# Kernel optimization log

Measured on AMD Instinct MI355X. Metric: run time of the kernel, lower is better.

Reference implementation:

```python
import jax, jax.numpy as jnp
import numpy as np

N = 100000      # nodes per type
E = 1600000     # edges per edge type
D = 128         # input feature dim
C = 128         # hidden channels (heads=1, concat)
DE = 16         # edge feature dim
OUT = 64        # out channels
L = 2           # num conv layers
T = 2           # num edge types: 0 = user->item, 1 = item->user


def setup_inputs() -> dict:
    key = jax.random.key(0)
    ks = jax.random.split(key, 17)
    s = 0.05  # keep attention logits / activations well-scaled
    return {
        "x_user": jax.random.normal(ks[0], (N, D), jnp.float32),
        "x_item": jax.random.normal(ks[1], (N, D), jnp.float32),
        "ea_ui": jax.random.normal(ks[2], (E, DE), jnp.float32),
        "ea_iu": jax.random.normal(ks[3], (E, DE), jnp.float32),
        "W_src": jax.random.normal(ks[4], (L, T, C, C), jnp.float32) * s,
        "W_dst": jax.random.normal(ks[5], (L, T, C, C), jnp.float32) * s,
        "W_edge": jax.random.normal(ks[6], (L, T, DE, C), jnp.float32) * s,
        "att_src": jax.random.normal(ks[7], (L, T, C), jnp.float32) * s,
        "att_dst": jax.random.normal(ks[8], (L, T, C), jnp.float32) * s,
        "att_edge": jax.random.normal(ks[9], (L, T, C), jnp.float32) * s,
        "conv_bias": jax.random.normal(ks[10], (L, T, C), jnp.float32) * s,
        "lin0_W": jax.random.normal(ks[11], (2, C, C), jnp.float32) * s,
        "lin0_b": jax.random.normal(ks[12], (2, C), jnp.float32) * s,
        "lin1_W": jax.random.normal(ks[13], (2, C, OUT), jnp.float32) * s,
        "lin1_b": jax.random.normal(ks[14], (2, OUT), jnp.float32) * s,
        "ei_ui": jax.random.randint(ks[15], (2, E), 0, N, jnp.int32),
        "ei_iu": jax.random.randint(ks[16], (2, E), 0, N, jnp.int32),
    }


def _gat_conv(x_src, x_dst, ei, ea, Ws, Wd, We, a_s, a_d, a_e, b):
    """PyG GATConv((-1,-1), C, heads=1, edge_dim=DE, add_self_loops=False)."""
    row, col = ei[0], ei[1]
    hs = x_src @ Ws                      # [Ns, C]
    hd = x_dst @ Wd                      # [Nd, C]
    he = ea @ We                         # [E, C]
    a = hs @ a_s                         # [Ns] alpha_src per source node
    adst = hd @ a_d                      # [Nd] alpha_dst per dest node
    ae = he @ a_e                        # [E]
    alpha = jax.nn.leaky_relu(a[row] + adst[col] + ae, 0.2)  # [E]
    n_dst = x_dst.shape[0]
    m = jax.ops.segment_max(alpha, col, num_segments=n_dst)  # stable softmax max
    ex = jnp.exp(alpha - m[col])
    den = jax.ops.segment_sum(ex, col, num_segments=n_dst)
    w = ex / den[col]                    # edge-softmax over incoming edges
    out = jax.ops.segment_sum(w[:, None] * hs[row], col, num_segments=n_dst)
    return out + b                       # [Nd, C]


def reference(x_user, x_item, ea_ui, ea_iu, W_src, W_dst, W_edge, att_src,
              att_dst, att_edge, conv_bias, lin0_W, lin0_b, lin1_W, lin1_b,
              ei_ui, ei_iu):
    xu, xi = x_user, x_item
    for l in range(L):
        # edge type 0: user -> item ; edge type 1: item -> user
        new_item = _gat_conv(xu, xi, ei_ui, ea_ui, W_src[l, 0], W_dst[l, 0],
                             W_edge[l, 0], att_src[l, 0], att_dst[l, 0],
                             att_edge[l, 0], conv_bias[l, 0])
        new_user = _gat_conv(xi, xu, ei_iu, ea_iu, W_src[l, 1], W_dst[l, 1],
                             W_edge[l, 1], att_src[l, 1], att_dst[l, 1],
                             att_edge[l, 1], conv_bias[l, 1])
        # HeteroConv aggr='sum' has one contribution per dst type; then relu
        xu = jax.nn.relu(new_user)
        xi = jax.nn.relu(new_item)
    # HeteroDictLinear stack (no activation between, per gnn.Sequential spec)
    xu = (xu @ lin0_W[0] + lin0_b[0]) @ lin1_W[0] + lin1_b[0]
    xi = (xi @ lin0_W[1] + lin0_b[1]) @ lin1_W[1] + lin1_b[1]
    return xu, xi
```

## Files before the change

### kernel.cpp

```cpp
#include <hip/hip_runtime.h>
#include <hip/hip_fp16.h>


typedef _Float16 half4 __attribute__((ext_vector_type(4)));
typedef float f32x4 __attribute__((ext_vector_type(4)));

#define KCAP 48

__device__ __forceinline__ float wave_sum(float v){
#pragma unroll
  for (int off = 32; off; off >>= 1) v += __shfl_xor(v, off);
  return v;
}

__global__ __launch_bounds__(64) void precompute_vec_kernel(
    const float* __restrict__ Wsrc, const float* __restrict__ Wdst,
    const float* __restrict__ Wedge, const float* __restrict__ As,
    const float* __restrict__ Ad, const float* __restrict__ Ae,
    float* __restrict__ pv_as, float* __restrict__ pv_ad, float* __restrict__ pv_ae)
{
  int b = blockIdx.x;
  int lt = b / 272, rem = b - lt * 272;
  int lane = threadIdx.x;
  const float* W; const float* a; float* out;
  if (rem < 128)      { W = Wsrc  + lt*16384 + rem*128;       a = As + lt*128; out = pv_as + lt*128 + rem; }
  else if (rem < 256) { int d = rem-128; W = Wdst + lt*16384 + d*128; a = Ad + lt*128; out = pv_ad + lt*128 + d; }
  else                { int j = rem-256; W = Wedge + lt*2048 + j*128; a = Ae + lt*128; out = pv_ae + lt*16 + j; }
  float s = W[lane]*a[lane] + W[lane+64]*a[lane+64];
  s = wave_sum(s);
  if (lane == 0) *out = s;
}

__global__ void combine_linear_kernel(const float* __restrict__ lin0W, const float* __restrict__ lin0b,
                                      const float* __restrict__ lin1W, const float* __restrict__ lin1b,
                                      float* __restrict__ Wc, float* __restrict__ bc)
{
  int idx = blockIdx.x * 256 + threadIdx.x;
  if (idx < 2*128*64) {
    int t = idx / 8192; int r = (idx / 64) & 127; int o = idx & 63;
    const float* w0 = lin0W + t*16384 + r*128;
    const float* w1 = lin1W + t*8192 + o;
    float s = 0.f;
    for (int m = 0; m < 128; ++m) s += w0[m] * w1[m*64];
    Wc[idx] = s;
  } else if (idx < 2*128*64 + 128) {
    int q = idx - 16384; int t = q >> 6; int o = q & 63;
    const float* b0 = lin0b + t*128;
    const float* w1 = lin1W + t*8192 + o;
    float s = lin1b[t*64 + o];
    for (int m = 0; m < 128; ++m) s += b0[m] * w1[m*64];
    bc[q] = s;
  }
}

__global__ __launch_bounds__(256) void wfrag_prep_kernel(
    const float* __restrict__ Wsrc, const float* __restrict__ pv_as,
    const float* __restrict__ pv_ad, const float* __restrict__ Wc,
    _Float16* __restrict__ Wf_conv, _Float16* __restrict__ Wf_mlp)
{
  int idx = blockIdx.x * 256 + threadIdx.x;
  if (idx < 73728) {
    int within = idx & 255;
    int l = within >> 2, i = within & 3;
    int rest = idx >> 8;
    int c = rest % 9; int rest2 = rest / 9;
    int s = rest2 & 7; int g = rest2 >> 3;
    int lg = g >> 1, who = g & 1;
    int k = s*16 + ((l>>4)<<2) + i;
    float val = 0.f;
    if (c < 8) {
      int col = c*16 + (l & 15);
      int lt = lg*2 + who;
      val = Wsrc[(size_t)lt*16384 + k*128 + col];
    } else {
      int cc = l & 15;
      if (cc == 0)      val = pv_as[(lg*2 + who)*128 + k];
      else if (cc == 1) val = pv_ad[(lg*2 + (who^1))*128 + k];
    }
    Wf_conv[idx] = (_Float16)val;
  } else {
    int q = idx - 73728;
    int within = q & 255;
    int l = within >> 2, i = within & 3;
    int rest = q >> 8;
    int c = rest & 3; int s = (rest >> 2) & 7; int m = rest >> 5;
    int k = s*16 + ((l>>4)<<2) + i;
    int col = c*16 + (l & 15);
    Wf_mlp[q] = (_Float16)Wc[m*8192 + k*64 + col];
  }
}

__device__ __forceinline__ void fill_body(
    int fid, int tid,
    const int* __restrict__ ei0, const int* __restrict__ ei1,
    const float* __restrict__ ea0, const float* __restrict__ ea1,
    const float* __restrict__ pv_ae,
    int* __restrict__ cnt0, int* __restrict__ cnt1,
    uint2* __restrict__ bkt0, uint2* __restrict__ bkt1, int E, int gEf)
{
  int type = (fid >= gEf) ? 1 : 0;
  const int* ei = type ? ei1 : ei0;
  const float* ea = type ? ea1 : ea0;
  int* cnt = type ? cnt1 : cnt0;
  uint2* bkt = type ? bkt1 : bkt0;
  int e = (fid - type * gEf) * 256 + tid;
  if (e >= E) return;
  int src = ei[e], col = ei[E + e];
  const float4* er = (const float4*)(ea + (size_t)e * 16);
  float4 a0 = er[0], a1 = er[1], a2 = er[2], a3 = er[3];
  const float* v0 = pv_ae + type * 16;
  const float* v1 = pv_ae + (2 + type) * 16;
  float ae0 = a0.x*v0[0] + a0.y*v0[1] + a0.z*v0[2] + a0.w*v0[3]
            + a1.x*v0[4] + a1.y*v0[5] + a1.z*v0[6] + a1.w*v0[7]
            + a2.x*v0[8] + a2.y*v0[9] + a2.z*v0[10] + a2.w*v0[11]
            + a3.x*v0[12] + a3.y*v0[13] + a3.z*v0[14] + a3.w*v0[15];
  float ae1 = a0.x*v1[0] + a0.y*v1[1] + a0.z*v1[2] + a0.w*v1[3]
            + a1.x*v1[4] + a1.y*v1[5] + a1.z*v1[6] + a1.w*v1[7]
            + a2.x*v1[8] + a2.y*v1[9] + a2.z*v1[10] + a2.w*v1[11]
            + a3.x*v1[12] + a3.y*v1[13] + a3.z*v1[14] + a3.w*v1[15];
  int pos = atomicAdd(&cnt[col], 1);
  if (pos < KCAP) {
    __half2 hh = __floats2half2_rn(ae0, ae1);
    uint2 val;
    val.x = (unsigned)src;
    val.y = *(const unsigned*)&hh;
    bkt[(size_t)col * KCAP + pos] = val;
  }
}

template<bool FIN, bool CONV>
__device__ __forceinline__ void gemm_body(_Float16* ldsb, int blk, int t,
    const void* __restrict__ Xv, const uint2* __restrict__ Wf,
    void* __restrict__ Hout, float* __restrict__ asrc, float* __restrict__ adst,
    const float* __restrict__ bias, int N)
{
  constexpr int NT = CONV ? 9 : 4;
  const int r0 = blk * 64;

  if (FIN) {
    const float* X = (const float*)Xv;
    for (int v = t; v < 2048; v += 256) {
      int row = v >> 5, q = v & 31;
      int r = r0 + row;
      float4 xv = make_float4(0.f, 0.f, 0.f, 0.f);
      if (r < N) xv = *(const float4*)(X + (size_t)r * 128 + q * 4);
      _Float16* d = &ldsb[row * 136 + q * 4];
      d[0] = (_Float16)xv.x; d[1] = (_Float16)xv.y;
      d[2] = (_Float16)xv.z; d[3] = (_Float16)xv.w;
    }
  } else {
    const _Float16* X = (const _Float16*)Xv;
    for (int v = t; v < 1024; v += 256) {
      int row = v >> 4, q = v & 15;
      int r = r0 + row;
      uint4 xv = make_uint4(0u, 0u, 0u, 0u);
      if (r < N) xv = *(const uint4*)(X + (size_t)r * 128 + q * 8);
      *(uint4*)(&ldsb[row * 136 + q * 8]) = xv;
    }
  }
  __syncthreads();

  const int w = t >> 6, l = t & 63;
  f32x4 acc[NT];
#pragma unroll
  for (int c = 0; c < NT; ++c) acc[c] = (f32x4)(0.f);

  const uint2* wp = Wf + l;
  const int aoff = (w * 16 + (l & 15)) * 136 + ((l >> 4) << 2);
#pragma unroll
  for (int s = 0; s < 8; ++s) {
    half4 af = *(const half4*)(&ldsb[aoff + s * 16]);
#pragma unroll
    for (int c = 0; c < NT; ++c) {
      uint2 bw = wp[(s * NT + c) * 64];
      half4 bf = *reinterpret_cast<const half4*>(&bw);
      acc[c] = __builtin_amdgcn_mfma_f32_16x16x16f16(af, bf, acc[c], 0, 0, 0);
    }
  }
  __syncthreads();

  if (CONV) {
#pragma unroll
    for (int c = 0; c < 8; ++c)
#pragma unroll
      for (int rg = 0; rg < 4; ++rg)
        ldsb[(w*16 + ((l>>4)<<2) + rg) * 136 + c*16 + (l & 15)] = (_Float16)acc[c][rg];
    if ((l & 15) < 2) {
      float* dst = ((l & 15) == 0) ? asrc : adst;
#pragma unroll
      for (int rg = 0; rg < 4; ++rg) {
        int r = r0 + w*16 + ((l>>4)<<2) + rg;
        if (r < N) dst[r] = acc[8][rg];
      }
    }
    __syncthreads();
    _Float16* H = (_Float16*)Hout;
    for (int v = t; v < 1024; v += 256) {
      int row = v >> 4, q = v & 15;
      int r = r0 + row;
      if (r < N)
        *(uint4*)(H + (size_t)r * 128 + q * 8) = *(const uint4*)(&ldsb[row * 136 + q * 8]);
    }
  } else {
    float* ldsf = (float*)ldsb;
#pragma unroll
    for (int c = 0; c < 4; ++c)
#pragma unroll
      for (int rg = 0; rg < 4; ++rg)
        ldsf[(w*16 + ((l>>4)<<2) + rg) * 68 + c*16 + (l & 15)] = acc[c][rg];
    __syncthreads();
    float* O = (float*)Hout;
    for (int v = t; v < 1024; v += 256) {
      int row = v >> 4, q = v & 15;
      int r = r0 + row;
      if (r < N) {
        float4 o = *(const float4*)(&ldsf[row * 68 + q * 4]);
        float4 bb = *(const float4*)(bias + q * 4);
        o.x += bb.x; o.y += bb.y; o.z += bb.z; o.w += bb.w;
        *(float4*)(O + (size_t)r * 64 + q * 4) = o;
      }
    }
  }
}

__global__ __launch_bounds__(256) void phase0_kernel(
    const float* __restrict__ xu, const float* __restrict__ xi,
    const uint2* __restrict__ Wfc,
    _Float16* __restrict__ hs_u, _Float16* __restrict__ hs_i,
    float* __restrict__ asrc_u, float* __restrict__ adst_u,
    float* __restrict__ asrc_i, float* __restrict__ adst_i,
    const int* __restrict__ ei0, const int* __restrict__ ei1,
    const float* __restrict__ ea0, const float* __restrict__ ea1,
    const float* __restrict__ pv_ae,
    int* __restrict__ cnt0, int* __restrict__ cnt1,
    uint2* __restrict__ bkt0, uint2* __restrict__ bkt1,
    int N, int E, int gB, int P, int gEf)
{
  __shared__ __align__(16) _Float16 ldsb[64 * 136];
  int b = blockIdx.x, t = threadIdx.x;
  int g = b / P, r = b - g * P;
  if (r == 0) {
    if (g < gB)
      gemm_body<true, true>(ldsb, g, t, xu, Wfc, hs_u, asrc_u, adst_u, nullptr, N);
    else
      gemm_body<true, true>(ldsb, g - gB, t, xi, Wfc + 4608, hs_i, asrc_i, adst_i, nullptr, N);
  } else {
    int fid = b - g - 1;
    if (fid < 2 * gEf)
      fill_body(fid, t, ei0, ei1, ea0, ea1, pv_ae, cnt0, cnt1, bkt0, bkt1, E, gEf);
  }
}

template<bool FIN, bool CONV>
__global__ __launch_bounds__(256) void gemm_pair_kernel(
    const void* __restrict__ X0, const void* __restrict__ X1,
    const uint2* __restrict__ Wf0, const uint2* __restrict__ Wf1,
    void* __restrict__ H0, void* __restrict__ H1,
    float* __restrict__ asrc0, float* __restrict__ adst0,
    float* __restrict__ asrc1, float* __restrict__ adst1,
    const float* __restrict__ bias0, const float* __restrict__ bias1,
    int N, int gB)
{
  __shared__ __align__(16) _Float16 ldsb[64 * 136];
  int b = blockIdx.x;
  if (b < gB)
    gemm_body<FIN, CONV>(ldsb, b, threadIdx.x, X0, Wf0, H0, asrc0, adst0, bias0, N);
  else
    gemm_body<FIN, CONV>(ldsb, b - gB, threadIdx.x, X1, Wf1, H1, asrc1, adst1, bias1, N);
}

__global__ __launch_bounds__(256) void aggregate_pair(
    const int* __restrict__ cnt0, const uint2* __restrict__ bkt0,
    const float* __restrict__ asrc0, const float* __restrict__ adst0,
    const __half2* __restrict__ hs0, const float* __restrict__ bias0,
    __half2* __restrict__ out0,
    const int* __restrict__ cnt1, const uint2* __restrict__ bkt1,
    const float* __restrict__ asrc1, const float* __restrict__ adst1,
    const __half2* __restrict__ hs1, const float* __restrict__ bias1,
    __half2* __restrict__ out1,
    int N, int lsel, int gHalf)
{
  int b = blockIdx.x;
  int tt = (b >= gHalf) ? 1 : 0;
  const int* cnt_tab = tt ? cnt1 : cnt0;
  const uint2* bkt   = tt ? bkt1 : bkt0;
  const float* asrc_tab = tt ? asrc1 : asrc0;
  const float* adst_tab = tt ? adst1 : adst0;
  const __half2* hs  = tt ? hs1 : hs0;
  const float* bias  = tt ? bias1 : bias0;
  __half2* xnew      = tt ? out1 : out0;

  int wid = threadIdx.x >> 6, lane = threadIdx.x & 63;
  int n = (b - tt * gHalf) * 4 + wid;
  if (n >= N) return;
  int cnt = cnt_tab[n]; if (cnt > KCAP) cnt = KCAP;
  float adst = adst_tab[n];
  int r = 0; float wgt = 0.f;
  if (lane < cnt) {
    uint2 sv = bkt[(size_t)n * KCAP + lane];
    r = (int)sv.x;
    __half2 hh = *(const __half2*)&sv.y;
    float ae = lsel ? __high2float(hh) : __low2float(hh);
    float a = asrc_tab[r];
    float al = a + adst + ae;
    al = (al > 0.f) ? al : 0.2f * al;
    wgt = __expf(al);
  }
  float den = wave_sum(wgt);
  float acc0 = 0.f, acc1 = 0.f;
  int k = 0;
  for (; k + 8 <= cnt; k += 8) {
    int rr[8]; float ww[8]; float2 f[8];
#pragma unroll
    for (int j = 0; j < 8; ++j) { rr[j] = __shfl(r, k + j); ww[j] = __shfl(wgt, k + j); }
#pragma unroll
    for (int j = 0; j < 8; ++j) f[j] = __half22float2(hs[(size_t)rr[j] * 64 + lane]);
#pragma unroll
    for (int j = 0; j < 8; ++j) { acc0 = fmaf(ww[j], f[j].x, acc0); acc1 = fmaf(ww[j], f[j].y, acc1); }
  }
  for (; k < cnt; ++k) {
    int rr = __shfl(r, k); float ww = __shfl(wgt, k);
    float2 f = __half22float2(hs[(size_t)rr * 64 + lane]);
    acc0 = fmaf(ww, f.x, acc0); acc1 = fmaf(ww, f.y, acc1);
  }
  float b0 = bias[2*lane], b1 = bias[2*lane + 1];
  float o0 = b0, o1 = b1;
  if (den > 0.f) {
    float inv = 1.f / den;
    o0 = fmaf(acc0, inv, b0);
    o1 = fmaf(acc1, inv, b1);
  }
  o0 = fmaxf(o0, 0.f);
  o1 = fmaxf(o1, 0.f);
  xnew[(size_t)n * 64 + lane] = __floats2half2_rn(o0, o1);
}

extern "C" void kernel_launch(void* const* d_in, const int* in_sizes, int n_in,
                              void* d_out, int out_size, void* d_ws, size_t ws_size,
                              hipStream_t stream)
{
  const float* x_user   = (const float*)d_in[0];
  const float* x_item   = (const float*)d_in[1];
  const float* ea_ui    = (const float*)d_in[2];
  const float* ea_iu    = (const float*)d_in[3];
  const float* W_src    = (const float*)d_in[4];
  const float* W_dst    = (const float*)d_in[5];
  const float* W_edge   = (const float*)d_in[6];
  const float* att_src  = (const float*)d_in[7];
  const float* att_dst  = (const float*)d_in[8];
  const float* att_edge = (const float*)d_in[9];
  const float* conv_bias= (const float*)d_in[10];
  const float* lin0W    = (const float*)d_in[11];
  const float* lin0b    = (const float*)d_in[12];
  const float* lin1W    = (const float*)d_in[13];
  const float* lin1b    = (const float*)d_in[14];
  const int*   ei_ui    = (const int*)d_in[15];
  const int*   ei_iu    = (const int*)d_in[16];

  const int N = in_sizes[0] / 128;
  const int E = in_sizes[15] / 2;

  char* p = (char*)d_ws;
  auto alloc = [&](size_t bytes) -> void* {
    void* r = (void*)p;
    p += (bytes + 255) & ~(size_t)255;
    return r;
  };
  _Float16* xu_a = (_Float16*)alloc((size_t)N * 128 * 2);
  _Float16* xi_a = (_Float16*)alloc((size_t)N * 128 * 2);
  _Float16* xu_b = (_Float16*)alloc((size_t)N * 128 * 2);
  _Float16* xi_b = (_Float16*)alloc((size_t)N * 128 * 2);
  _Float16* hs_u = (_Float16*)alloc((size_t)N * 128 * 2);
  _Float16* hs_i = (_Float16*)alloc((size_t)N * 128 * 2);
  uint2* bkt_ui  = (uint2*)alloc((size_t)N * KCAP * 8);
  uint2* bkt_iu  = (uint2*)alloc((size_t)N * KCAP * 8);
  int*   cnt_ui  = (int*)alloc((size_t)2 * N * 4);
  int*   cnt_iu  = cnt_ui + N;
  float* asrc_u  = (float*)alloc((size_t)N * 4);
  float* adst_u  = (float*)alloc((size_t)N * 4);
  float* asrc_i  = (float*)alloc((size_t)N * 4);
  float* adst_i  = (float*)alloc((size_t)N * 4);
  float* pv_as   = (float*)alloc(512 * 4);
  float* pv_ad   = (float*)alloc(512 * 4);
  float* pv_ae   = (float*)alloc(64 * 4);
  float* Wc      = (float*)alloc(2 * 128 * 64 * 4);
  float* bc      = (float*)alloc(128 * 4);
  _Float16* Wf_conv = (_Float16*)alloc(73728 * 2);
  _Float16* Wf_mlp  = (_Float16*)alloc(16384 * 2);

  precompute_vec_kernel<<<4 * 272, 64, 0, stream>>>(W_src, W_dst, W_edge,
      att_src, att_dst, att_edge, pv_as, pv_ad, pv_ae);
  combine_linear_kernel<<<65, 256, 0, stream>>>(lin0W, lin0b, lin1W, lin1b, Wc, bc);
  wfrag_prep_kernel<<<352, 256, 0, stream>>>(W_src, pv_as, pv_ad, Wc, Wf_conv, Wf_mlp);
  hipMemsetAsync(cnt_ui, 0, (size_t)2 * N * 4, stream);

  const int gEf = (E + 255) / 256;
  const int gB  = (N + 63) / 64;
  const int GB2 = 2 * gB;
  const int P   = 1 + (2 * gEf + GB2 - 1) / GB2;
  const int gN4 = (N + 3) / 4;
  const uint2* Wfc = (const uint2*)Wf_conv;
  const uint2* Wfm = (const uint2*)Wf_mlp;

  phase0_kernel<<<P * GB2, 256, 0, stream>>>(x_user, x_item, Wfc,
      hs_u, hs_i, asrc_u, adst_u, asrc_i, adst_i,
      ei_ui, ei_iu, ea_ui, ea_iu, pv_ae, cnt_ui, cnt_iu, bkt_ui, bkt_iu,
      N, E, gB, P, gEf);

  aggregate_pair<<<2 * gN4, 256, 0, stream>>>(
      cnt_ui, bkt_ui, asrc_u, adst_i, (const __half2*)hs_u, conv_bias + 0*128, (__half2*)xi_a,
      cnt_iu, bkt_iu, asrc_i, adst_u, (const __half2*)hs_i, conv_bias + 1*128, (__half2*)xu_a,
      N, 0, gN4);

  gemm_pair_kernel<false, true><<<GB2, 256, 0, stream>>>(
      xu_a, xi_a, Wfc + 2*4608, Wfc + 3*4608, hs_u, hs_i,
      asrc_u, adst_u, asrc_i, adst_i, nullptr, nullptr, N, gB);

  aggregate_pair<<<2 * gN4, 256, 0, stream>>>(
      cnt_ui, bkt_ui, asrc_u, adst_i, (const __half2*)hs_u, conv_bias + 2*128, (__half2*)xi_b,
      cnt_iu, bkt_iu, asrc_i, adst_u, (const __half2*)hs_i, conv_bias + 3*128, (__half2*)xu_b,
      N, 1, gN4);

  float* out = (float*)d_out;
  gemm_pair_kernel<false, false><<<GB2, 256, 0, stream>>>(
      xu_b, xi_b, Wfm, Wfm + 2048, out, out + (size_t)N * 64,
      nullptr, nullptr, nullptr, nullptr, bc, bc + 64, N, gB);
}
```

Before: 516.5 us.

## Two-pass partitioned edge bucketing to localize scatter atomics

Replaces the direct per-edge atomic scatter into destination buckets with a two-pass scheme. Edges are first binned by coarse destination partition (dst>>12) using LDS histograms and one global atomic per partition per block, and written to a staging buffer. A second kernel then scatters each partition's records into the per-node buckets, so the atomics and writes land in a localized address range. This adds a 16-byte staging record per edge, which costs extra memory traffic, plus an extra kernel launch. The per-partition capacity margin could drop edges on skewed graphs, and the order of edges within a bucket changes.

```diff
diff --git a/kernel.cpp b/kernel.cpp
--- a/kernel.cpp
+++ b/kernel.cpp
@@ -6,6 +6,7 @@
 typedef float f32x4 __attribute__((ext_vector_type(4)));
 
 #define KCAP 48
+#define PSHIFT 12
 
 __device__ __forceinline__ float wave_sum(float v){
 #pragma unroll
@@ -90,41 +91,82 @@
   }
 }
 
-__device__ __forceinline__ void fill_body(
-    int fid, int tid,
+__device__ __forceinline__ void fill1_body(
+    int fid, int tid, int* lds_i,
     const int* __restrict__ ei0, const int* __restrict__ ei1,
     const float* __restrict__ ea0, const float* __restrict__ ea1,
     const float* __restrict__ pv_ae,
-    int* __restrict__ cnt0, int* __restrict__ cnt1,
-    uint2* __restrict__ bkt0, uint2* __restrict__ bkt1, int E, int gEf)
+    int* __restrict__ gcur, uint4* __restrict__ stage,
+    int E, int gEf, int NP, int CAP)
 {
   int type = (fid >= gEf) ? 1 : 0;
   const int* ei = type ? ei1 : ei0;
   const float* ea = type ? ea1 : ea0;
-  int* cnt = type ? cnt1 : cnt0;
+  int e = (fid - type * gEf) * 256 + tid;
+  bool valid = e < E;
+  int src = 0, dst = 0, p = 0;
+  unsigned ae2 = 0;
+  if (valid) {
+    src = ei[e]; dst = ei[E + e];
+    const float4* er = (const float4*)(ea + (size_t)e * 16);
+    float4 a0 = er[0], a1 = er[1], a2 = er[2], a3 = er[3];
+    const float* v0 = pv_ae + type * 16;
+    const float* v1 = pv_ae + (2 + type) * 16;
+    float ae0 = a0.x*v0[0] + a0.y*v0[1] + a0.z*v0[2] + a0.w*v0[3]
+              + a1.x*v0[4] + a1.y*v0[5] + a1.z*v0[6] + a1.w*v0[7]
+              + a2.x*v0[8] + a2.y*v0[9] + a2.z*v0[10] + a2.w*v0[11]
+              + a3.x*v0[12] + a3.y*v0[13] + a3.z*v0[14] + a3.w*v0[15];
+    float ae1 = a0.x*v1[0] + a0.y*v1[1] + a0.z*v1[2] + a0.w*v1[3]
+              + a1.x*v1[4] + a1.y*v1[5] + a1.z*v1[6] + a1.w*v1[7]
+              + a2.x*v1[8] + a2.y*v1[9] + a2.z*v1[10] + a2.w*v1[11]
+              + a3.x*v1[12] + a3.y*v1[13] + a3.z*v1[14] + a3.w*v1[15];
+    __half2 hh = __floats2half2_rn(ae0, ae1);
+    ae2 = *(const unsigned*)&hh;
+    p = dst >> PSHIFT;
+  }
+  int* h     = lds_i;
+  int* basep = lds_i + 32;
+  if (tid < NP) h[tid] = 0;
+  __syncthreads();
+  int rank = 0;
+  if (valid) rank = atomicAdd(&h[p], 1);
+  __syncthreads();
+  if (tid < NP) {
+    int c = h[tid];
+    basep[tid] = (c > 0) ? atomicAdd(&gcur[type * NP + tid], c) : 0;
+  }
+  __syncthreads();
+  if (valid) {
+    int idx = basep[p] + rank;
+    if (idx < CAP) {
+      uint4 rec;
+      rec.x = (unsigned)src; rec.y = (unsigned)dst; rec.z = ae2; rec.w = 0u;
+      stage[(size_t)(type * NP + p) * CAP + idx] = rec;
+    }
+  }
+}
+
+__global__ __launch_bounds__(256) void scatter2_kernel(
+    const uint4* __restrict__ stage, const int* __restrict__ gcur,
+    int* __restrict__ cnt0, int* __restrict__ cnt1,
+    uint2* __restrict__ bkt0, uint2* __restrict__ bkt1,
+    int NP, int CAP, int BPP)
+{
+  int pid = blockIdx.x / BPP;
+  int j   = blockIdx.x - pid * BPP;
+  int count = gcur[pid];
+  if (count > CAP) count = CAP;
+  int i = j * 256 + threadIdx.x;
+  if (i >= count) return;
+  uint4 rec = stage[(size_t)pid * CAP + i];
+  int type = (pid >= NP) ? 1 : 0;
+  int dst = (int)rec.y;
+  int* cnt  = type ? cnt1 : cnt0;
   uint2* bkt = type ? bkt1 : bkt0;
-  int e = (fid - type * gEf) * 256 + tid;
-  if (e >= E) return;
-  int src = ei[e], col = ei[E + e];
-  const float4* er = (const float4*)(ea + (size_t)e * 16);
-  float4 a0 = er[0], a1 = er[1], a2 = er[2], a3 = er[3];
-  const float* v0 = pv_ae + type * 16;
-  const float* v1 = pv_ae + (2 + type) * 16;
-  float ae0 = a0.x*v0[0] + a0.y*v0[1] + a0.z*v0[2] + a0.w*v0[3]
-            + a1.x*v0[4] + a1.y*v0[5] + a1.z*v0[6] + a1.w*v0[7]
-            + a2.x*v0[8] + a2.y*v0[9] + a2.z*v0[10] + a2.w*v0[11]
-            + a3.x*v0[12] + a3.y*v0[13] + a3.z*v0[14] + a3.w*v0[15];
-  float ae1 = a0.x*v1[0] + a0.y*v1[1] + a0.z*v1[2] + a0.w*v1[3]
-            + a1.x*v1[4] + a1.y*v1[5] + a1.z*v1[6] + a1.w*v1[7]
-            + a2.x*v1[8] + a2.y*v1[9] + a2.z*v1[10] + a2.w*v1[11]
-            + a3.x*v1[12] + a3.y*v1[13] + a3.z*v1[14] + a3.w*v1[15];
-  int pos = atomicAdd(&cnt[col], 1);
+  int pos = atomicAdd(&cnt[dst], 1);
   if (pos < KCAP) {
-    __half2 hh = __floats2half2_rn(ae0, ae1);
-    uint2 val;
-    val.x = (unsigned)src;
-    val.y = *(const unsigned*)&hh;
-    bkt[(size_t)col * KCAP + pos] = val;
+    uint2 v; v.x = rec.x; v.y = rec.z;
+    bkt[(size_t)dst * KCAP + pos] = v;
   }
 }
 
@@ -232,9 +274,8 @@
     const int* __restrict__ ei0, const int* __restrict__ ei1,
     const float* __restrict__ ea0, const float* __restrict__ ea1,
     const float* __restrict__ pv_ae,
-    int* __restrict__ cnt0, int* __restrict__ cnt1,
-    uint2* __restrict__ bkt0, uint2* __restrict__ bkt1,
-    int N, int E, int gB, int P, int gEf)
+    int* __restrict__ gcur, uint4* __restrict__ stage,
+    int N, int E, int gB, int P, int gEf, int NP, int CAP)
 {
   __shared__ __align__(16) _Float16 ldsb[64 * 136];
   int b = blockIdx.x, t = threadIdx.x;
@@ -247,7 +288,7 @@
   } else {
     int fid = b - g - 1;
     if (fid < 2 * gEf)
-      fill_body(fid, t, ei0, ei1, ea0, ea1, pv_ae, cnt0, cnt1, bkt0, bkt1, E, gEf);
+      fill1_body(fid, t, (int*)ldsb, ei0, ei1, ea0, ea1, pv_ae, gcur, stage, E, gEf, NP, CAP);
   }
 }
 
@@ -360,6 +401,11 @@
   const int N = in_sizes[0] / 128;
   const int E = in_sizes[15] / 2;
 
+  const int NP  = (N + (1 << PSHIFT) - 1) >> PSHIFT;
+  int CAPr = (int)(((long long)E << PSHIFT) / N) + 8192;
+  const int CAP = (CAPr + 255) & ~255;
+  const int BPP = CAP / 256;
+
   char* p = (char*)d_ws;
   auto alloc = [&](size_t bytes) -> void* {
     void* r = (void*)p;
@@ -374,8 +420,10 @@
   _Float16* hs_i = (_Float16*)alloc((size_t)N * 128 * 2);
   uint2* bkt_ui  = (uint2*)alloc((size_t)N * KCAP * 8);
   uint2* bkt_iu  = (uint2*)alloc((size_t)N * KCAP * 8);
-  int*   cnt_ui  = (int*)alloc((size_t)2 * N * 4);
+  int*   cnt_ui  = (int*)alloc(((size_t)2 * N + 64) * 4);
   int*   cnt_iu  = cnt_ui + N;
+  int*   gcur    = cnt_ui + 2 * N;
+  uint4* stage   = (uint4*)alloc((size_t)2 * NP * CAP * 16);
   float* asrc_u  = (float*)alloc((size_t)N * 4);
   float* adst_u  = (float*)alloc((size_t)N * 4);
   float* asrc_i  = (float*)alloc((size_t)N * 4);
@@ -392,7 +440,7 @@
       att_src, att_dst, att_edge, pv_as, pv_ad, pv_ae);
   combine_linear_kernel<<<65, 256, 0, stream>>>(lin0W, lin0b, lin1W, lin1b, Wc, bc);
   wfrag_prep_kernel<<<352, 256, 0, stream>>>(W_src, pv_as, pv_ad, Wc, Wf_conv, Wf_mlp);
-  hipMemsetAsync(cnt_ui, 0, (size_t)2 * N * 4, stream);
+  hipMemsetAsync(cnt_ui, 0, ((size_t)2 * N + 64) * 4, stream);
 
   const int gEf = (E + 255) / 256;
   const int gB  = (N + 63) / 64;
@@ -404,8 +452,11 @@
 
   phase0_kernel<<<P * GB2, 256, 0, stream>>>(x_user, x_item, Wfc,
       hs_u, hs_i, asrc_u, adst_u, asrc_i, adst_i,
-      ei_ui, ei_iu, ea_ui, ea_iu, pv_ae, cnt_ui, cnt_iu, bkt_ui, bkt_iu,
-      N, E, gB, P, gEf);
+      ei_ui, ei_iu, ea_ui, ea_iu, pv_ae, gcur, stage,
+      N, E, gB, P, gEf, NP, CAP);
+
+  scatter2_kernel<<<2 * NP * BPP, 256, 0, stream>>>(stage, gcur,
+      cnt_ui, cnt_iu, bkt_ui, bkt_iu, NP, CAP, BPP);
 
   aggregate_pair<<<2 * gN4, 256, 0, stream>>>(
       cnt_ui, bkt_ui, asrc_u, adst_i, (const __half2*)hs_u, conv_bias + 0*128, (__half2*)xi_a,
```

After: 678.7 us. 31.4% more time.
